# Performance work log

Hardware: AMD Instinct MI355X
Metric: run time of the kernel (lower is better)

## Reference

```python
import jax, jax.numpy as jnp
import numpy as np

D_MODEL = 1024
NGRAM = 2
SHIFT_STEP = 1


def induction_head(ids, hidden, ngram=NGRAM, shift_step=SHIFT_STEP):
    # ids: [B, S] int, hidden: [B, S, D]
    B, S = ids.shape
    eq = ids[:, None, :] == ids[:, :, None]                      # [B, S, S]
    causal = jnp.tril(jnp.ones((S, S), dtype=bool), k=-1)        # strictly lower
    m = jnp.logical_and(eq, causal)
    acc = m
    cur = m
    for _ in range(1, ngram):
        # F.pad(cur, (1,-1,1,-1)): shift down-right by 1 on the [S,S] dims
        cur = jnp.pad(cur, ((0, 0), (1, 0), (1, 0)))[:, :S, :S]
        acc = jnp.logical_and(acc, cur)                          # stack+sum>=ngram == AND
    ih = acc
    if shift_step > 0:
        # F.pad(ih, (shift,-shift)): shift right by shift_step on last dim
        ih = jnp.pad(ih, ((0, 0), (0, 0), (shift_step, 0)))[:, :, :S]
    ih = jnp.logical_and(ih, causal)
    ihf = ih.astype(hidden.dtype)
    denom = jnp.sum(ihf, axis=2, keepdims=True)
    norm = jnp.where(denom > 0, ihf / jnp.where(denom > 0, denom, 1), 0)  # nan_to_num(0)
    return jnp.einsum('bmn,bnz->bmz', norm, hidden)


def setup_inputs() -> dict:
    key = jax.random.key(0)
    k1, k2, k3, k4, k5, k6 = jax.random.split(key, 6)
    B, S, D = 4, 2048, D_MODEL
    x = jax.random.normal(k1, (B, S, D), dtype=jnp.float32)
    input_ids = jax.random.randint(k2, (B, S), 0, 512, dtype=jnp.int64)
    s = 1.0 / np.sqrt(D)
    W0 = jax.random.uniform(k3, (D, D), jnp.float32, -s, s)
    b0 = jax.random.uniform(k4, (D,), jnp.float32, -s, s)
    W1 = jax.random.uniform(k5, (D, D), jnp.float32, -s, s)
    b1 = jax.random.uniform(k6, (D,), jnp.float32, -s, s)
    return {"x": x, "input_ids": input_ids, "W0": W0, "b0": b0, "W1": W1, "b1": b1}


def reference(x, input_ids, W0, b0, W1, b1):
    h0 = induction_head(input_ids, x, ngram=NGRAM)
    h1 = x
    y = h0 @ W0.T + b0 + (h1 @ W1.T + b1)
    return y
```

## Files before the change

### kernel.cpp

```cpp
#include <hip/hip_runtime.h>
#include <hip/hip_bf16.h>

#define BATCH   4
#define S_LEN   2048
#define DMODEL  1024
#define M_TOT   (BATCH * S_LEN)
#define N_TOT   DMODEL
#define K_TOT   DMODEL

#define MAXR    2048
#define RSLOTS  256

#define CNT_OFF   0
#define ROWS_OFF  1024
#define AVG_OFF   16384
#define XBF_OFF   (10u * 1024u * 1024u)
#define WBF_OFF   (27u * 1024u * 1024u)
#define FULL_NEED (30u * 1024u * 1024u)
#define MID_NEED  (9u * 1024u * 1024u)

typedef __attribute__((ext_vector_type(8))) short bf16x8;
typedef __attribute__((ext_vector_type(4))) short bf16x4v;
typedef __attribute__((ext_vector_type(4))) float f32x4;

__device__ __forceinline__ short f2bf(float f) {
  union { float f; unsigned int u; } v; v.f = f;
  unsigned int u = v.u;
  u += 0x7fffu + ((u >> 16) & 1u);
  return (short)(u >> 16);
}

#define GLOAD(gp, lp)                                               \
  __builtin_amdgcn_global_load_lds(                                 \
      (const __attribute__((address_space(1))) void*)(gp),          \
      (__attribute__((address_space(3))) void*)(lp), 16, 0, 0)

__global__ void init_kernel(int* __restrict__ cnt) {
  if (threadIdx.x == 0) *cnt = 0;
}

#define NX8 (M_TOT * K_TOT / 8)
#define NW8 (N_TOT * K_TOT / 8)
__global__ __launch_bounds__(256) void cvt2_kernel(
    const float* __restrict__ x, short* __restrict__ xo,
    const float* __restrict__ w, short* __restrict__ wo) {
  int idx = blockIdx.x * 256 + threadIdx.x;
  const float* in; short* out; int k;
  if (idx < NX8)             { in = x; out = xo; k = idx; }
  else if (idx < NX8 + NW8)  { in = w; out = wo; k = idx - NX8; }
  else return;
  const float4* p = (const float4*)in + (size_t)k * 2;
  float4 a = p[0], b = p[1];
  bf16x8 v = { f2bf(a.x), f2bf(a.y), f2bf(a.z), f2bf(a.w),
               f2bf(b.x), f2bf(b.y), f2bf(b.z), f2bf(b.w) };
  *(bf16x8*)(out + (size_t)k * 8) = v;
}

__global__ __launch_bounds__(256) void gemm_bf16_kernel(
    const short* __restrict__ Ab, const short* __restrict__ Bb,
    const float* __restrict__ b0, const float* __restrict__ b1,
    float* __restrict__ C) {
  __shared__ short As[2][128 * 32];
  __shared__ short Bs[2][128 * 32];

  const int tid  = threadIdx.x;
  const int lane = tid & 63;
  const int w    = tid >> 6;
  const int wm   = w >> 1, wn = w & 1;

  const int swz = (blockIdx.x & 7) * 64 + (blockIdx.x >> 3);
  const int bn  = swz & 7, bm = swz >> 3;

  const int l15 = lane & 15;
  const int kc  = (lane >> 4) << 3;

  const short* Abase = Ab + (size_t)bm * 128 * K_TOT;
  const short* Bbase = Bb + (size_t)bn * 128 * K_TOT;

  const int srow = tid >> 2;
  const int scol = (tid & 3) << 3;
  const int lbase = (tid & ~63) * 8;

  f32x4 acc[4][4];
#pragma unroll
  for (int a = 0; a < 4; a++)
#pragma unroll
    for (int b = 0; b < 4; b++) {
      f32x4 z = {0.f, 0.f, 0.f, 0.f};
      acc[a][b] = z;
    }

#define STG(buf, k0)                                                        \
  {                                                                         \
    _Pragma("unroll")                                                       \
    for (int q = 0; q < 2; ++q) {                                           \
      GLOAD(Abase + (size_t)(q * 64 + srow) * K_TOT + (k0) + scol,          \
            &As[buf][q * 2048 + lbase]);                                    \
      GLOAD(Bbase + (size_t)(q * 64 + srow) * K_TOT + (k0) + scol,          \
            &Bs[buf][q * 2048 + lbase]);                                    \
    }                                                                       \
  }

  STG(0, 0);
  __syncthreads();

  const int NT = K_TOT / 32;
  for (int t = 0; t < NT; ++t) {
    const int cur = t & 1;
    if (t + 1 < NT) STG(cur ^ 1, (t + 1) * 32);

    bf16x8 af[4], bb[4];
#pragma unroll
    for (int mi = 0; mi < 4; ++mi)
      af[mi] = *(const bf16x8*)&As[cur][(wm * 64 + mi * 16 + l15) * 32 + kc];
#pragma unroll
    for (int ni = 0; ni < 4; ++ni)
      bb[ni] = *(const bf16x8*)&Bs[cur][(wn * 64 + ni * 16 + l15) * 32 + kc];

#pragma unroll
    for (int mi = 0; mi < 4; ++mi)
#pragma unroll
      for (int ni = 0; ni < 4; ++ni)
        acc[mi][ni] = __builtin_amdgcn_mfma_f32_16x16x32_bf16(
            af[mi], bb[ni], acc[mi][ni], 0, 0, 0);

    __syncthreads();
  }
#undef STG

#pragma unroll
  for (int ni = 0; ni < 4; ni++) {
    const int col = bn * 128 + wn * 64 + ni * 16 + l15;
    const float bias = b0[col] + b1[col];
#pragma unroll
    for (int mi = 0; mi < 4; mi++) {
      const int row0 = bm * 128 + wm * 64 + mi * 16 + ((lane >> 4) << 2);
#pragma unroll
      for (int r = 0; r < 4; r++)
        C[(size_t)(row0 + r) * N_TOT + col] = acc[mi][ni][r] + bias;
    }
  }
}

#define BM 128
#define BN 128
#define BK 32
#define LDK 40

__global__ __launch_bounds__(256) void gemm_bias_kernel(
    const float* __restrict__ A, const float* __restrict__ Bw,
    const float* __restrict__ b0, const float* __restrict__ b1,
    float* __restrict__ C) {
  __shared__ short As[2][BM][LDK];
  __shared__ short Bs[2][BM][LDK];

  const int tid  = threadIdx.x;
  const int lane = tid & 63;
  const int w    = tid >> 6;
  const int wm   = w >> 1, wn = w & 1;
  const int bn   = blockIdx.x & 7;
  const int bm   = blockIdx.x >> 3;
  const int l15 = lane & 15;
  const int kc  = (lane >> 4) << 3;

  f32x4 acc[4][4];
#pragma unroll
  for (int a = 0; a < 4; a++)
#pragma unroll
    for (int b = 0; b < 4; b++) {
      f32x4 z = {0.f, 0.f, 0.f, 0.f};
      acc[a][b] = z;
    }

  const float* Abase = A  + (size_t)bm * BM * K_TOT;
  const float* Bbase = Bw + (size_t)bn * BN * K_TOT;
  float4 ra[4], rb[4];

#define LOADT(k0)                                                          \
  {                                                                        \
    _Pragma("unroll")                                                      \
    for (int q = 0; q < 4; q++) {                                          \
      int fidx = tid + q * 256;                                            \
      int r = fidx >> 3, cc = (fidx & 7) << 2;                             \
      ra[q] = *(const float4*)(Abase + (size_t)r * K_TOT + (k0) + cc);     \
      rb[q] = *(const float4*)(Bbase + (size_t)r * K_TOT + (k0) + cc);     \
    }                                                                      \
  }
#define STORET(buf)                                                        \
  {                                                                        \
    _Pragma("unroll")                                                      \
    for (int q = 0; q < 4; q++) {                                          \
      int fidx = tid + q * 256;                                            \
      int r = fidx >> 3, cc = (fidx & 7) << 2;                             \
      bf16x4v av = { f2bf(ra[q].x), f2bf(ra[q].y),                         \
                     f2bf(ra[q].z), f2bf(ra[q].w) };                       \
      bf16x4v bv = { f2bf(rb[q].x), f2bf(rb[q].y),                         \
                     f2bf(rb[q].z), f2bf(rb[q].w) };                       \
      *(bf16x4v*)&As[buf][r][cc] = av;                                     \
      *(bf16x4v*)&Bs[buf][r][cc] = bv;                                     \
    }                                                                      \
  }

  LOADT(0);
  STORET(0);
  __syncthreads();

  const int NT = K_TOT / BK;
  for (int t = 0; t < NT; ++t) {
    const int cur = t & 1;
    if (t + 1 < NT) LOADT((t + 1) * BK);
    bf16x8 af[4], bf_[4];
#pragma unroll
    for (int mi = 0; mi < 4; mi++)
      af[mi] = *(const bf16x8*)&As[cur][wm * 64 + mi * 16 + l15][kc];
#pragma unroll
    for (int ni = 0; ni < 4; ni++)
      bf_[ni] = *(const bf16x8*)&Bs[cur][wn * 64 + ni * 16 + l15][kc];
#pragma unroll
    for (int mi = 0; mi < 4; mi++)
#pragma unroll
      for (int ni = 0; ni < 4; ni++)
        acc[mi][ni] = __builtin_amdgcn_mfma_f32_16x16x32_bf16(
            af[mi], bf_[ni], acc[mi][ni], 0, 0, 0);
    if (t + 1 < NT) STORET(cur ^ 1);
    __syncthreads();
  }
#undef LOADT
#undef STORET

#pragma unroll
  for (int ni = 0; ni < 4; ni++) {
    const int col = bn * BN + wn * 64 + ni * 16 + l15;
    const float bias = b0[col] + b1[col];
#pragma unroll
    for (int mi = 0; mi < 4; mi++) {
      const int row0 = bm * BM + wm * 64 + mi * 16 + ((lane >> 4) << 2);
#pragma unroll
      for (int r = 0; r < 4; r++)
        C[(size_t)(row0 + r) * N_TOT + col] = acc[mi][ni][r] + bias;
    }
  }
}

__global__ __launch_bounds__(256) void scan_kernel(
    const int* __restrict__ ids, const float* __restrict__ x,
    int* __restrict__ cnt, int* __restrict__ rows, float* __restrict__ avg,
    const float* __restrict__ W0, float* __restrict__ y) {
  const int b = blockIdx.x >> 11;
  const int i = blockIdx.x & (S_LEN - 1);
  if (i < 3) return;

  const int* idb = ids + b * S_LEN;
  __shared__ int   s_cnt;
  __shared__ int   s_slot;
  __shared__ int   s_list[S_LEN];
  __shared__ float s_avg[DMODEL];

  const int tid = threadIdx.x;
  if (tid == 0) s_cnt = 0;
  __syncthreads();

  const int ti = idb[i], tp = idb[i - 1];
  for (int j = 2 + tid; j < i; j += 256) {
    if (idb[j - 1] == ti && idb[j - 2] == tp) {
      int p = atomicAdd(&s_cnt, 1);
      s_list[p] = j;
    }
  }
  __syncthreads();
  const int c = s_cnt;
  if (c == 0) return;

  float4 s = {0.f, 0.f, 0.f, 0.f};
  const float4* xb = (const float4*)(x + (size_t)b * S_LEN * DMODEL);
  for (int r = 0; r < c; ++r) {
    const int j = s_list[r];
    float4 v = xb[(size_t)j * (DMODEL / 4) + tid];
    s.x += v.x; s.y += v.y; s.z += v.z; s.w += v.w;
  }
  const float inv = 1.0f / (float)c;
  s.x *= inv; s.y *= inv; s.z *= inv; s.w *= inv;

  if (tid == 0) s_slot = atomicAdd(cnt, 1);
  __syncthreads();
  const int slot = s_slot;

  if (slot < MAXR) {
    if (tid == 0) rows[slot] = b * S_LEN + i;
    *(float4*)(avg + (size_t)slot * DMODEL + tid * 4) = s;
  } else {
    *(float4*)&s_avg[tid * 4] = s;
    __syncthreads();
    float* yrow = y + ((size_t)(b * S_LEN + i)) * DMODEL;
#pragma unroll
    for (int q = 0; q < 4; ++q) {
      const int n = q * 256 + tid;
      const float4* wr = (const float4*)(W0 + (size_t)n * DMODEL);
      float a = 0.f;
      for (int kk = 0; kk < DMODEL / 4; ++kk) {
        float4 wv = wr[kk];
        float4 av = *(const float4*)&s_avg[kk * 4];
        a += wv.x * av.x + wv.y * av.y + wv.z * av.z + wv.w * av.w;
      }
      atomicAdd(&yrow[n], a);
    }
  }
}

__global__ __launch_bounds__(256) void apply_kernel(
    const int* __restrict__ cnt, const int* __restrict__ rows,
    const float* __restrict__ avg, const float* __restrict__ W0,
    float* __restrict__ y) {
  int R = *cnt; if (R > MAXR) R = MAXR;
  const int rslot = blockIdx.x >> 4;
  if (rslot >= R) return;
  const int cg = blockIdx.x & 15;
  const int tid = threadIdx.x;

  __shared__ float s_avg[DMODEL];

  for (int r = rslot; r < R; r += RSLOTS) {
    if (r != rslot) __syncthreads();
    *(float4*)&s_avg[tid * 4] =
        *(const float4*)(avg + (size_t)r * DMODEL + tid * 4);
    __syncthreads();

    const int n  = cg * 64 + (tid >> 2);
    const int ks = (tid & 3) * 256;
    const float4* wr = (const float4*)(W0 + (size_t)n * DMODEL + ks);
    const float4* ar = (const float4*)&s_avg[ks];
    float a = 0.f;
#pragma unroll 8
    for (int u = 0; u < 64; ++u) {
      float4 wv = wr[u], av = ar[u];
      a += wv.x * av.x + wv.y * av.y + wv.z * av.z + wv.w * av.w;
    }
    a += __shfl_down(a, 1, 4);
    a += __shfl_down(a, 2, 4);
    if ((tid & 3) == 0) {
      const int m = rows[r];
      y[(size_t)m * DMODEL + n] += a;
    }
  }
}

__global__ __launch_bounds__(256) void induct_kernel(
    const int* __restrict__ ids, const float* __restrict__ x,
    const float* __restrict__ W0, float* __restrict__ y) {
  const int b = blockIdx.x >> 11;
  const int i = blockIdx.x & (S_LEN - 1);
  if (i < 3) return;
  const int* idb = ids + b * S_LEN;
  __shared__ int   s_cnt;
  __shared__ int   s_list[S_LEN];
  __shared__ float s_avg[DMODEL];
  const int tid = threadIdx.x;
  if (tid == 0) s_cnt = 0;
  __syncthreads();
  const int ti = idb[i], tp = idb[i - 1];
  for (int j = 2 + tid; j < i; j += 256) {
    if (idb[j - 1] == ti && idb[j - 2] == tp) {
      int p = atomicAdd(&s_cnt, 1);
      s_list[p] = j;
    }
  }
  __syncthreads();
  const int c = s_cnt;
  if (c == 0) return;
  float4 s = {0.f, 0.f, 0.f, 0.f};
  const float4* xb = (const float4*)(x + (size_t)b * S_LEN * DMODEL);
  for (int r = 0; r < c; ++r) {
    const int j = s_list[r];
    float4 v = xb[(size_t)j * (DMODEL / 4) + tid];
    s.x += v.x; s.y += v.y; s.z += v.z; s.w += v.w;
  }
  const float inv = 1.0f / (float)c;
  s.x *= inv; s.y *= inv; s.z *= inv; s.w *= inv;
  *(float4*)&s_avg[tid * 4] = s;
  __syncthreads();
  float out[4];
#pragma unroll
  for (int q = 0; q < 4; ++q) {
    const int n = q * 256 + tid;
    const float4* wr = (const float4*)(W0 + (size_t)n * DMODEL);
    float a = 0.f;
    for (int kk = 0; kk < DMODEL / 4; ++kk) {
      float4 wv = wr[kk];
      float4 av = *(const float4*)&s_avg[kk * 4];
      a += wv.x * av.x + wv.y * av.y + wv.z * av.z + wv.w * av.w;
    }
    out[q] = a;
  }
  float* yrow = y + ((size_t)(b * S_LEN + i)) * DMODEL;
#pragma unroll
  for (int q = 0; q < 4; ++q) yrow[q * 256 + tid] += out[q];
}

extern "C" void kernel_launch(void* const* d_in, const int* in_sizes, int n_in,
                              void* d_out, int out_size, void* d_ws, size_t ws_size,
                              hipStream_t stream) {
  const float* x   = (const float*)d_in[0];
  const int*   ids = (const int*)  d_in[1];
  const float* W0  = (const float*)d_in[2];
  const float* b0  = (const float*)d_in[3];
  const float* W1  = (const float*)d_in[4];
  const float* b1  = (const float*)d_in[5];
  float* y = (float*)d_out;

  char* ws = (char*)d_ws;
  int*   cnt  = (int*)(ws + CNT_OFF);
  int*   rows = (int*)(ws + ROWS_OFF);
  float* avg  = (float*)(ws + AVG_OFF);
  short* xbf  = (short*)(ws + XBF_OFF);
  short* wbf  = (short*)(ws + WBF_OFF);

  const bool full = ws_size >= FULL_NEED;
  const bool mid  = ws_size >= MID_NEED;

  if (full) {
    cvt2_kernel<<<(NX8 + NW8 + 255) / 256, 256, 0, stream>>>(x, xbf, W1, wbf);
    gemm_bf16_kernel<<<(M_TOT / 128) * (N_TOT / 128), 256, 0, stream>>>(xbf, wbf, b0, b1, y);
  } else {
    gemm_bias_kernel<<<(M_TOT / BM) * (N_TOT / BN), 256, 0, stream>>>(x, W1, b0, b1, y);
  }

  if (mid) {
    init_kernel<<<1, 64, 0, stream>>>(cnt);
    scan_kernel<<<BATCH * S_LEN, 256, 0, stream>>>(ids, x, cnt, rows, avg, W0, y);
    apply_kernel<<<RSLOTS * 16, 256, 0, stream>>>(cnt, rows, avg, W0, y);
  } else {
    induct_kernel<<<BATCH * S_LEN, 256, 0, stream>>>(ids, x, W0, y);
  }
}
```

Measured before the change: 146.6 us.

## Replace per-row scan with bigram-key match scan and separate gather kernel

```diff
diff --git a/kernel.cpp b/kernel.cpp
--- a/kernel.cpp
+++ b/kernel.cpp
@@ -14,6 +14,7 @@
 #define CNT_OFF   0
 #define ROWS_OFF  1024
 #define AVG_OFF   16384
+#define KEYS_OFF  (8704u * 1024u)
 #define XBF_OFF   (10u * 1024u * 1024u)
 #define WBF_OFF   (27u * 1024u * 1024u)
 #define FULL_NEED (30u * 1024u * 1024u)
@@ -242,68 +243,90 @@
   }
 }
 
-__global__ __launch_bounds__(256) void scan_kernel(
-    const int* __restrict__ ids, const float* __restrict__ x,
-    int* __restrict__ cnt, int* __restrict__ rows, float* __restrict__ avg,
-    const float* __restrict__ W0, float* __restrict__ y) {
-  const int b = blockIdx.x >> 11;
-  const int i = blockIdx.x & (S_LEN - 1);
-  if (i < 3) return;
-
+__global__ __launch_bounds__(1024) void scan2_kernel(
+    const int* __restrict__ ids, int* __restrict__ cnt,
+    int* __restrict__ rows, int* __restrict__ keybuf) {
+  const int b = blockIdx.x;
   const int* idb = ids + b * S_LEN;
-  __shared__ int   s_cnt;
-  __shared__ int   s_slot;
-  __shared__ int   s_list[S_LEN];
-  __shared__ float s_avg[DMODEL];
-
+  __shared__ int s_ids[S_LEN];
+  __shared__ __align__(16) int keys[S_LEN];
   const int tid = threadIdx.x;
-  if (tid == 0) s_cnt = 0;
-  __syncthreads();
-
-  const int ti = idb[i], tp = idb[i - 1];
-  for (int j = 2 + tid; j < i; j += 256) {
-    if (idb[j - 1] == ti && idb[j - 2] == tp) {
-      int p = atomicAdd(&s_cnt, 1);
-      s_list[p] = j;
-    }
-  }
-  __syncthreads();
-  const int c = s_cnt;
-  if (c == 0) return;
-
-  float4 s = {0.f, 0.f, 0.f, 0.f};
-  const float4* xb = (const float4*)(x + (size_t)b * S_LEN * DMODEL);
-  for (int r = 0; r < c; ++r) {
-    const int j = s_list[r];
-    float4 v = xb[(size_t)j * (DMODEL / 4) + tid];
-    s.x += v.x; s.y += v.y; s.z += v.z; s.w += v.w;
-  }
-  const float inv = 1.0f / (float)c;
-  s.x *= inv; s.y *= inv; s.z *= inv; s.w *= inv;
-
-  if (tid == 0) s_slot = atomicAdd(cnt, 1);
-  __syncthreads();
-  const int slot = s_slot;
-
-  if (slot < MAXR) {
-    if (tid == 0) rows[slot] = b * S_LEN + i;
+
+#pragma unroll
+  for (int h = 0; h < 2; ++h) {
+    int i = tid + h * 1024;
+    s_ids[i] = idb[i];
+  }
+  __syncthreads();
+#pragma unroll
+  for (int h = 0; h < 2; ++h) {
+    int i = tid + h * 1024;
+    keys[i] = (i > 0) ? (s_ids[i - 1] * 512 + s_ids[i]) : -1;
+  }
+  __syncthreads();
+#pragma unroll
+  for (int h = 0; h < 2; ++h) {
+    int i = tid + h * 1024;
+    keybuf[b * S_LEN + i] = keys[i];
+  }
+
+  const int4* k4 = (const int4*)keys;
+#pragma unroll
+  for (int h = 0; h < 2; ++h) {
+    const int i = tid + h * 1024;
+    if (i >= 3) {
+      const int ki = keys[i];
+      const int pmax = i - 2;
+      int c = 0;
+      for (int q = 0; q * 4 <= pmax; ++q) {
+        int4 kk = k4[q];
+        int p0 = q * 4;
+        c += (p0     >= 1 && p0     <= pmax && kk.x == ki);
+        c += (p0 + 1 >= 1 && p0 + 1 <= pmax && kk.y == ki);
+        c += (p0 + 2 <= pmax && kk.z == ki);
+        c += (p0 + 3 <= pmax && kk.w == ki);
+      }
+      if (c > 0) {
+        int slot = atomicAdd(cnt, 1);
+        if (slot < MAXR) rows[slot] = b * S_LEN + i;
+      }
+    }
+  }
+}
+
+__global__ __launch_bounds__(256) void gather_kernel(
+    const int* __restrict__ cnt, const int* __restrict__ rows,
+    const int* __restrict__ keybuf, const float* __restrict__ x,
+    float* __restrict__ avg) {
+  int R = *cnt; if (R > MAXR) R = MAXR;
+  const int tid = threadIdx.x;
+  __shared__ int s_cnt;
+  __shared__ int s_list[S_LEN];
+
+  for (int slot = blockIdx.x; slot < R; slot += RSLOTS) {
+    if (tid == 0) s_cnt = 0;
+    __syncthreads();
+
+    const int row = rows[slot];
+    const int b = row >> 11, i = row & (S_LEN - 1);
+    const int* kb = keybuf + b * S_LEN;
+    const int ki = kb[i];
+    for (int p = 1 + tid; p <= i - 2; p += 256)
+      if (kb[p] == ki) { int q = atomicAdd(&s_cnt, 1); s_list[q] = p + 1; }
+    __syncthreads();
+
+    const int c = s_cnt;
+    float4 s = {0.f, 0.f, 0.f, 0.f};
+    const float4* xb = (const float4*)(x + (size_t)b * S_LEN * DMODEL);
+    for (int r = 0; r < c; ++r) {
+      const int j = s_list[r];
+      float4 v = xb[(size_t)j * (DMODEL / 4) + tid];
+      s.x += v.x; s.y += v.y; s.z += v.z; s.w += v.w;
+    }
+    const float inv = 1.0f / (float)c;
+    s.x *= inv; s.y *= inv; s.z *= inv; s.w *= inv;
     *(float4*)(avg + (size_t)slot * DMODEL + tid * 4) = s;
-  } else {
-    *(float4*)&s_avg[tid * 4] = s;
-    __syncthreads();
-    float* yrow = y + ((size_t)(b * S_LEN + i)) * DMODEL;
-#pragma unroll
-    for (int q = 0; q < 4; ++q) {
-      const int n = q * 256 + tid;
-      const float4* wr = (const float4*)(W0 + (size_t)n * DMODEL);
-      float a = 0.f;
-      for (int kk = 0; kk < DMODEL / 4; ++kk) {
-        float4 wv = wr[kk];
-        float4 av = *(const float4*)&s_avg[kk * 4];
-        a += wv.x * av.x + wv.y * av.y + wv.z * av.z + wv.w * av.w;
-      }
-      atomicAdd(&yrow[n], a);
-    }
+    __syncthreads();
   }
 }
 
@@ -411,11 +434,18 @@
   int*   cnt  = (int*)(ws + CNT_OFF);
   int*   rows = (int*)(ws + ROWS_OFF);
   float* avg  = (float*)(ws + AVG_OFF);
+  int*   keyb = (int*)(ws + KEYS_OFF);
   short* xbf  = (short*)(ws + XBF_OFF);
   short* wbf  = (short*)(ws + WBF_OFF);
 
   const bool full = ws_size >= FULL_NEED;
   const bool mid  = ws_size >= MID_NEED;
+
+  if (mid) {
+    init_kernel<<<1, 64, 0, stream>>>(cnt);
+    scan2_kernel<<<BATCH, 1024, 0, stream>>>(ids, cnt, rows, keyb);
+    gather_kernel<<<RSLOTS, 256, 0, stream>>>(cnt, rows, keyb, x, avg);
+  }
 
   if (full) {
     cvt2_kernel<<<(NX8 + NW8 + 255) / 256, 256, 0, stream>>>(x, xbf, W1, wbf);
@@ -425,8 +455,6 @@
   }
 
   if (mid) {
-    init_kernel<<<1, 64, 0, stream>>>(cnt);
-    scan_kernel<<<BATCH * S_LEN, 256, 0, stream>>>(ids, x, cnt, rows, avg, W0, y);
     apply_kernel<<<RSLOTS * 16, 256, 0, stream>>>(cnt, rows, avg, W0, y);
   } else {
     induct_kernel<<<BATCH * S_LEN, 256, 0, stream>>>(ids, x, W0, y);
```

Result: slower. 216.7 us (+47.8%).
